# Kernel tuning notes

Hardware: AMD Instinct MI355X
Metric: run time of the kernel (lower is better)

Reference implementation:

```python
import jax, jax.numpy as jnp
import numpy as np
from jax import lax

C = 64          # grid_channels
RGB = 3         # rgb_channels
D = 128         # conditioning_dim
NUM_CLASSES = 1000
HIDDEN = 256    # hypernet hidden
NUM_STEPS = 32
TOT1 = C * C * 9


def setup_inputs() -> dict:
    key = jax.random.key(0)
    ks = jax.random.split(key, 20)
    s = 0.02
    B, H, W = 32, 64, 64
    return {
        "class_labels": jax.random.randint(ks[0], (B,), 0, NUM_CLASSES),
        "initial_grid": jax.random.normal(ks[1], (B, C, H, W), jnp.float32) * 0.1,
        "emb": jax.random.normal(ks[2], (NUM_CLASSES, D), jnp.float32) * s,
        "hw1": jax.random.normal(ks[3], (D, HIDDEN), jnp.float32) * s,
        "hb1": jnp.zeros((HIDDEN,), jnp.float32),
        "hw2": jax.random.normal(ks[4], (HIDDEN, HIDDEN), jnp.float32) * s,
        "hb2": jnp.zeros((HIDDEN,), jnp.float32),
        "hw3": jax.random.normal(ks[5], (HIDDEN, 2 * TOT1), jnp.float32) * s,
        "hb3": jnp.zeros((2 * TOT1,), jnp.float32),
        "f1w1": jax.random.normal(ks[6], (D, D), jnp.float32) * s,
        "f1b1": jnp.zeros((D,), jnp.float32),
        "f1w2": jax.random.normal(ks[7], (D, 2 * C), jnp.float32) * s,
        "f1b2": jnp.concatenate([jnp.ones((C,), jnp.float32), jnp.zeros((C,), jnp.float32)]),
        "f2w1": jax.random.normal(ks[8], (D, D), jnp.float32) * s,
        "f2b1": jnp.zeros((D,), jnp.float32),
        "f2w2": jax.random.normal(ks[9], (D, 2 * C), jnp.float32) * s,
        "f2b2": jnp.concatenate([jnp.ones((C,), jnp.float32), jnp.zeros((C,), jnp.float32)]),
        "blend": jnp.float32(0.5),
    }


def _conv_circ_one(x, w):
    # x: [C,H,W], w: [Cout,Cin,3,3]; circular pad then VALID conv == padding=1 circular
    xp = jnp.pad(x, ((0, 0), (1, 1), (1, 1)), mode='wrap')
    return lax.conv_general_dilated(xp[None], w, (1, 1), 'VALID')[0]

_bconv = jax.vmap(_conv_circ_one)  # per-sample dynamic weights over batch


def _film_params(cond, w1, b1, w2, b2):
    p = jax.nn.relu(cond @ w1 + b1) @ w2 + b2  # [B, 2C]
    return p[:, :C, None, None], p[:, C:, None, None]


def reference(class_labels, initial_grid, emb, hw1, hb1, hw2, hb2, hw3, hb3,
              f1w1, f1b1, f1w2, f1b2, f2w1, f2b1, f2w2, f2b2, blend):
    cond = emb[class_labels]                       # [B, D]
    h = jax.nn.relu(cond @ hw1 + hb1)
    h = jax.nn.relu(h @ hw2 + hb2)
    weights = h @ hw3 + hb3                        # [B, 2*C*C*9]
    B = cond.shape[0]
    w1 = weights[:, :TOT1].reshape(B, C, C, 3, 3)
    w2 = weights[:, TOT1:].reshape(B, C, C, 3, 3)
    g1, be1 = _film_params(cond, f1w1, f1b1, f1w2, f1b2)
    g2, be2 = _film_params(cond, f2w1, f2b1, f2w2, f2b2)
    blend_s = jax.nn.sigmoid(blend)

    def step(grid, _):
        u = jax.nn.relu(g1 * _bconv(grid, w1) + be1)
        u = jax.nn.relu(g2 * _bconv(u, w2) + be2)
        grid = (1 - blend_s) * grid + blend_s * u
        rgb = jax.nn.sigmoid(grid[:, :RGB])
        return grid, rgb

    _, traj = lax.scan(step, initial_grid, None, length=NUM_STEPS)  # [T,B,3,H,W]
    return traj[-1], traj
```

## Files before the change

kernel.cpp:

```cpp
#include <hip/hip_runtime.h>


typedef __attribute__((ext_vector_type(8))) short short8;
typedef __attribute__((ext_vector_type(4))) float f32x4;
typedef __attribute__((ext_vector_type(8))) unsigned short us8;

__device__ __forceinline__ unsigned short f2bf(float f) {
  unsigned int u = __builtin_bit_cast(unsigned int, f);
  u = (u + 0x7FFFu + ((u >> 16) & 1u)) >> 16;
  return (unsigned short)u;
}
__device__ __forceinline__ float bf2f(unsigned short h) {
  unsigned int u = ((unsigned int)h) << 16;
  return __builtin_bit_cast(float, u);
}

__device__ __forceinline__ void gl_lds16(const void* g, void* l) {
  __builtin_amdgcn_global_load_lds((const __attribute__((address_space(1))) void*)g,
                                   (__attribute__((address_space(3))) void*)l, 16, 0, 0);
}

__global__ void hyper_kernel(const int* __restrict__ labels, const float* __restrict__ emb,
                             const float* __restrict__ hw1, const float* __restrict__ hb1,
                             const float* __restrict__ hw2, const float* __restrict__ hb2,
                             float* __restrict__ h2T) {
  __shared__ float cond[128];
  __shared__ float h1[256];
  const int s = blockIdx.x, j = threadIdx.x;
  if (j < 128) cond[j] = emb[(size_t)labels[s] * 128 + j];
  __syncthreads();
  float a = hb1[j];
  for (int k = 0; k < 128; ++k) a += cond[k] * hw1[k * 256 + j];
  h1[j] = fmaxf(a, 0.f);
  __syncthreads();
  float a2 = hb2[j];
  for (int k = 0; k < 256; ++k) a2 += h1[k] * hw2[k * 256 + j];
  h2T[j * 32 + s] = fmaxf(a2, 0.f);
}

__global__ void film_kernel(const int* __restrict__ labels, const float* __restrict__ emb,
                            const float* __restrict__ f1w1, const float* __restrict__ f1b1,
                            const float* __restrict__ f1w2, const float* __restrict__ f1b2,
                            const float* __restrict__ f2w1, const float* __restrict__ f2b1,
                            const float* __restrict__ f2w2, const float* __restrict__ f2b2,
                            float* __restrict__ film) {
  __shared__ float cond[128];
  __shared__ float hid[128];
  const int s = blockIdx.x, which = blockIdx.y, j = threadIdx.x;
  const float* W1 = which ? f2w1 : f1w1;
  const float* B1 = which ? f2b1 : f1b1;
  const float* W2 = which ? f2w2 : f1w2;
  const float* B2 = which ? f2b2 : f1b2;
  cond[j] = emb[(size_t)labels[s] * 128 + j];
  __syncthreads();
  float a = B1[j];
  for (int k = 0; k < 128; ++k) a += cond[k] * W1[k * 128 + j];
  hid[j] = fmaxf(a, 0.f);
  __syncthreads();
  float p = B2[j];
  for (int k = 0; k < 128; ++k) p += hid[k] * W2[k * 128 + j];
  film[(size_t)((which * 2 + (j >> 6)) * 32 + s) * 64 + (j & 63)] = p;
}

__launch_bounds__(256)
__global__ void wgen_kernel(const float* __restrict__ h2T, const float* __restrict__ hw3,
                            const float* __restrict__ hb3, unsigned short* __restrict__ W) {
  __shared__ float h2l[8192];
  const int t = threadIdx.x;
  for (int i = t; i < 8192; i += 256) h2l[i] = h2T[i];
  __syncthreads();
  const int j  = blockIdx.x * 64 + (t & 63);
  const int sg = t >> 6;
  float acc[8];
  #pragma unroll
  for (int i = 0; i < 8; ++i) acc[i] = 0.f;
  const float* hp = &h2l[sg * 8];
  #pragma unroll 4
  for (int k = 0; k < 256; ++k) {
    const float w = hw3[(size_t)k * 73728 + j];
    const float4 hA = *(const float4*)(hp + k * 32);
    const float4 hB = *(const float4*)(hp + k * 32 + 4);
    acc[0] += hA.x * w; acc[1] += hA.y * w; acc[2] += hA.z * w; acc[3] += hA.w * w;
    acc[4] += hB.x * w; acc[5] += hB.y * w; acc[6] += hB.z * w; acc[7] += hB.w * w;
  }
  const float bias = hb3[j];
  const int cv = j / 36864;
  const int r  = j - cv * 36864;
  const int co = r / 576;
  const int r2 = r - co * 576;
  const int ci = r2 / 9;
  const int tap = r2 - ci * 9;
  const int sw = (co * 64 + ci) ^ ((co & 7) << 3);
  #pragma unroll
  for (int i = 0; i < 8; ++i) {
    const int s2 = sg * 8 + i;
    W[(size_t)((s2 * 2 + cv) * 9 + tap) * 4096 + sw] = f2bf(acc[i] + bias);
  }
}

__global__ void init_kernel(const float* __restrict__ gin, unsigned short* __restrict__ g0) {
  __shared__ float lds[64][65];
  const int b = blockIdx.x >> 6, y = blockIdx.x & 63;
  const int t = threadIdx.x;
  {
    const int ci = t >> 2, xq = t & 3;
    const float* base = gin + (size_t)((b * 64 + ci) * 64 + y) * 64;
    #pragma unroll
    for (int q = 0; q < 4; ++q) {
      const int x0 = (xq + q * 4) * 4;
      const float4 v = *(const float4*)(base + x0);
      lds[ci][x0+0] = v.x; lds[ci][x0+1] = v.y; lds[ci][x0+2] = v.z; lds[ci][x0+3] = v.w;
    }
  }
  __syncthreads();
  const int x = t >> 2, cq = t & 3, ci0 = cq * 16;
  us8 lo, hi;
  #pragma unroll
  for (int i = 0; i < 8; ++i) lo[i] = f2bf(lds[ci0 + i][x]);
  #pragma unroll
  for (int i = 0; i < 8; ++i) hi[i] = f2bf(lds[ci0 + 8 + i][x]);
  char* dbase = (char*)(g0 + (size_t)(b * 64 + y) * 4096);
  const int o = x * 128 + ci0 * 2, sw = (x & 7) << 4;
  *(us8*)(dbase + (o ^ sw)) = lo;
  *(us8*)(dbase + ((o + 16) ^ sw)) = hi;
}

template<int WHICH>
__launch_bounds__(512, 2)
__global__ void conv_kernel(const unsigned short* __restrict__ Wall,
                            const unsigned short* __restrict__ src,
                            unsigned short* __restrict__ dst,
                            const unsigned short* __restrict__ gold,
                            const float* __restrict__ film,
                            const float* __restrict__ blendp,
                            float* __restrict__ out, int t) {
  __shared__ unsigned short in_lds[10 * 4096];
  __shared__ unsigned short w_lds[9 * 4096];
  const int tid  = threadIdx.x;
  const int wid  = tid >> 6;
  const int lane = tid & 63;
  const int l15  = lane & 15;
  const int lhi  = lane >> 4;
  const int s    = blockIdx.x >> 3;
  const int y0   = (blockIdx.x & 7) * 8;

  const unsigned short* srcs = src + (size_t)s * 262144;
  const unsigned short* Wb   = Wall + (size_t)((s * 2 + WHICH) * 9) * 4096;

  #pragma unroll
  for (int q = 0; q < 10; ++q) {
    const int c   = q * 8 + wid;
    const int row = c >> 3, part = c & 7;
    const int gy  = (y0 + row + 63) & 63;
    gl_lds16(srcs + gy * 4096 + part * 512 + lane * 8, &in_lds[row * 4096 + part * 512]);
  }
  #pragma unroll
  for (int q = 0; q < 9; ++q) {
    const int c = q * 8 + wid;
    gl_lds16(Wb + c * 512 + lane * 8, &w_lds[c * 512]);
  }
  asm volatile("s_waitcnt vmcnt(0)" ::: "memory");
  __syncthreads();

  f32x4 acc[4][4];
  #pragma unroll
  for (int m = 0; m < 4; ++m)
    #pragma unroll
    for (int n = 0; n < 4; ++n)
      #pragma unroll
      for (int j = 0; j < 4; ++j) acc[m][n][j] = 0.f;

  #pragma unroll
  for (int tap = 0; tap < 9; ++tap) {
    const int ky = tap / 3, kx = tap % 3;
    short8 af[4][2], bfr[4][2];
    #pragma unroll
    for (int m = 0; m < 4; ++m) {
      const int co = m * 16 + l15;
      #pragma unroll
      for (int kk = 0; kk < 2; ++kk) {
        const int off = tap * 8192 + ((co * 128 + kk * 64 + lhi * 16) ^ ((co & 7) << 4));
        af[m][kk] = *(const short8*)((const char*)w_lds + off);
      }
    }
    const int r = wid + ky;
    #pragma unroll
    for (int n = 0; n < 4; ++n) {
      const int xs = (n * 16 + l15 + kx + 63) & 63;
      #pragma unroll
      for (int kk = 0; kk < 2; ++kk) {
        const int off = r * 8192 + ((xs * 128 + kk * 64 + lhi * 16) ^ ((xs & 7) << 4));
        bfr[n][kk] = *(const short8*)((const char*)in_lds + off);
      }
    }
    #pragma unroll
    for (int kk = 0; kk < 2; ++kk)
      #pragma unroll
      for (int m = 0; m < 4; ++m)
        #pragma unroll
        for (int n = 0; n < 4; ++n)
          acc[m][n] = __builtin_amdgcn_mfma_f32_16x16x32_bf16(af[m][kk], bfr[n][kk], acc[m][n], 0, 0, 0);
  }

  const int y = y0 + wid;
  const float* fg = film + WHICH * 2 * 2048;
  const float* fb = fg + 2048;
  float bs = 0.f, obs = 0.f;
  if (WHICH == 1) { bs = 1.f / (1.f + expf(-blendp[0])); obs = 1.f - bs; }
  unsigned short* drow = dst + (size_t)s * 262144 + y * 4096;
  const unsigned short* grow = (WHICH == 1) ? (gold + (size_t)s * 262144 + y * 4096) : (const unsigned short*)nullptr;

  #pragma unroll
  for (int m = 0; m < 4; ++m) {
    const int co0 = m * 16 + lhi * 4;
    const float4 g  = *(const float4*)&fg[s * 64 + co0];
    const float4 be = *(const float4*)&fb[s * 64 + co0];
    #pragma unroll
    for (int n = 0; n < 4; ++n) {
      const int x = n * 16 + l15;
      const int off = (x * 128 + co0 * 2) ^ ((x & 7) << 4);
      const f32x4 v = acc[m][n];
      const float u0 = fmaxf(g.x * v[0] + be.x, 0.f);
      const float u1 = fmaxf(g.y * v[1] + be.y, 0.f);
      const float u2 = fmaxf(g.z * v[2] + be.z, 0.f);
      const float u3 = fmaxf(g.w * v[3] + be.w, 0.f);
      if (WHICH == 0) {
        ushort4 pk; pk.x = f2bf(u0); pk.y = f2bf(u1); pk.z = f2bf(u2); pk.w = f2bf(u3);
        *(ushort4*)((char*)drow + off) = pk;
      } else {
        const ushort4 od = *(const ushort4*)((const char*)grow + off);
        const float g0 = obs * bf2f(od.x) + bs * u0;
        const float g1 = obs * bf2f(od.y) + bs * u1;
        const float g2 = obs * bf2f(od.z) + bs * u2;
        const float g3 = obs * bf2f(od.w) + bs * u3;
        ushort4 pk; pk.x = f2bf(g0); pk.y = f2bf(g1); pk.z = f2bf(g2); pk.w = f2bf(g3);
        *(ushort4*)((char*)drow + off) = pk;
        if (co0 == 0) {
          const float r0 = 1.f / (1.f + expf(-g0));
          const float r1 = 1.f / (1.f + expf(-g1));
          const float r2 = 1.f / (1.f + expf(-g2));
          float* ob = out + 393216 + (size_t)((t * 32 + s) * 3) * 4096 + y * 64 + x;
          ob[0] = r0; ob[4096] = r1; ob[8192] = r2;
          if (t == 31) {
            float* o2 = out + (size_t)(s * 3) * 4096 + y * 64 + x;
            o2[0] = r0; o2[4096] = r1; o2[8192] = r2;
          }
        }
      }
    }
  }
}

extern "C" void kernel_launch(void* const* d_in, const int* in_sizes, int n_in,
                              void* d_out, int out_size, void* d_ws, size_t ws_size,
                              hipStream_t stream) {
  (void)in_sizes; (void)n_in; (void)out_size; (void)ws_size;
  const int*   labels = (const int*)d_in[0];
  const float* gin    = (const float*)d_in[1];
  const float* emb    = (const float*)d_in[2];
  const float* hw1    = (const float*)d_in[3];
  const float* hb1    = (const float*)d_in[4];
  const float* hw2    = (const float*)d_in[5];
  const float* hb2    = (const float*)d_in[6];
  const float* hw3    = (const float*)d_in[7];
  const float* hb3    = (const float*)d_in[8];
  const float* f1w1   = (const float*)d_in[9];
  const float* f1b1   = (const float*)d_in[10];
  const float* f1w2   = (const float*)d_in[11];
  const float* f1b2   = (const float*)d_in[12];
  const float* f2w1   = (const float*)d_in[13];
  const float* f2b1   = (const float*)d_in[14];
  const float* f2w2   = (const float*)d_in[15];
  const float* f2b2   = (const float*)d_in[16];
  const float* blend  = (const float*)d_in[17];
  float* out = (float*)d_out;

  char* ws = (char*)d_ws;
  unsigned short* grid0 = (unsigned short*)(ws + (size_t)0);
  unsigned short* grid1 = (unsigned short*)(ws + (size_t)16777216);
  unsigned short* ubuf  = (unsigned short*)(ws + (size_t)33554432);
  unsigned short* Wbuf  = (unsigned short*)(ws + (size_t)50331648);
  float* h2T  = (float*)(ws + (size_t)55050240);
  float* film = (float*)(ws + (size_t)55083008);

  hyper_kernel<<<32, 256, 0, stream>>>(labels, emb, hw1, hb1, hw2, hb2, h2T);
  film_kernel<<<dim3(32, 2), 128, 0, stream>>>(labels, emb, f1w1, f1b1, f1w2, f1b2,
                                               f2w1, f2b1, f2w2, f2b2, film);
  wgen_kernel<<<1152, 256, 0, stream>>>(h2T, hw3, hb3, Wbuf);
  init_kernel<<<2048, 256, 0, stream>>>(gin, grid0);

  for (int t = 0; t < 32; ++t) {
    unsigned short* gi = (t & 1) ? grid1 : grid0;
    unsigned short* go = (t & 1) ? grid0 : grid1;
    conv_kernel<0><<<256, 512, 0, stream>>>(Wbuf, gi, ubuf, nullptr, film, nullptr, nullptr, t);
    conv_kernel<1><<<256, 512, 0, stream>>>(Wbuf, ubuf, go, gi, film, blend, out, t);
  }
}
```

Measured before the change: 1.430 ms.

## Double-buffer conv tap fragments, software-pipeline wgen loads, remap conv block order

The conv kernel now loads the LDS fragments for the next tap into a second register set while MFMAs run on the current tap, and raises wave priority around the MFMA block. The wgen kernel has each thread compute two output columns with float2 loads and a four-deep register prefetch of hw3 rows, which halves the grid size. Conv blocks are also remapped so that consecutive block IDs cover different samples instead of different row bands of one sample. The register pressure from the extra fragment buffers could reduce occupancy under the 512x2 launch bounds.

```diff
diff --git a/kernel.cpp b/kernel.cpp
--- a/kernel.cpp
+++ b/kernel.cpp
@@ -69,32 +69,78 @@
   const int t = threadIdx.x;
   for (int i = t; i < 8192; i += 256) h2l[i] = h2T[i];
   __syncthreads();
-  const int j  = blockIdx.x * 64 + (t & 63);
-  const int sg = t >> 6;
-  float acc[8];
-  #pragma unroll
-  for (int i = 0; i < 8; ++i) acc[i] = 0.f;
-  const float* hp = &h2l[sg * 8];
-  #pragma unroll 4
-  for (int k = 0; k < 256; ++k) {
-    const float w = hw3[(size_t)k * 73728 + j];
-    const float4 hA = *(const float4*)(hp + k * 32);
-    const float4 hB = *(const float4*)(hp + k * 32 + 4);
-    acc[0] += hA.x * w; acc[1] += hA.y * w; acc[2] += hA.z * w; acc[3] += hA.w * w;
-    acc[4] += hB.x * w; acc[5] += hB.y * w; acc[6] += hB.z * w; acc[7] += hB.w * w;
-  }
-  const float bias = hb3[j];
-  const int cv = j / 36864;
-  const int r  = j - cv * 36864;
-  const int co = r / 576;
-  const int r2 = r - co * 576;
-  const int ci = r2 / 9;
-  const int tap = r2 - ci * 9;
-  const int sw = (co * 64 + ci) ^ ((co & 7) << 3);
-  #pragma unroll
-  for (int i = 0; i < 8; ++i) {
-    const int s2 = sg * 8 + i;
-    W[(size_t)((s2 * 2 + cv) * 9 + tap) * 4096 + sw] = f2bf(acc[i] + bias);
+  const int lane = t & 63, sg = t >> 6;
+  const int j0 = blockIdx.x * 128 + lane * 2;
+  const float* __restrict__ gp = hw3 + j0;
+  const float* __restrict__ hp = h2l + sg * 8;
+
+  float acc[16];
+  #pragma unroll
+  for (int i = 0; i < 16; ++i) acc[i] = 0.f;
+
+  float2 bA[8], bB[8], bC[8], bD[8];
+  #pragma unroll
+  for (int u = 0; u < 8; ++u) bA[u] = *(const float2*)(gp + (size_t)(u) * 73728);
+  #pragma unroll
+  for (int u = 0; u < 8; ++u) bB[u] = *(const float2*)(gp + (size_t)(8 + u) * 73728);
+  #pragma unroll
+  for (int u = 0; u < 8; ++u) bC[u] = *(const float2*)(gp + (size_t)(16 + u) * 73728);
+
+#define WG_COMPUTE(BUF, KB)                                                    \
+  _Pragma("unroll")                                                            \
+  for (int u = 0; u < 8; ++u) {                                                \
+    const float4 hA = *(const float4*)(hp + ((KB) + u) * 32);                  \
+    const float4 hB = *(const float4*)(hp + ((KB) + u) * 32 + 4);              \
+    const float2 wv = BUF[u];                                                  \
+    acc[0]  += hA.x * wv.x; acc[1]  += hA.x * wv.y;                            \
+    acc[2]  += hA.y * wv.x; acc[3]  += hA.y * wv.y;                            \
+    acc[4]  += hA.z * wv.x; acc[5]  += hA.z * wv.y;                            \
+    acc[6]  += hA.w * wv.x; acc[7]  += hA.w * wv.y;                            \
+    acc[8]  += hB.x * wv.x; acc[9]  += hB.x * wv.y;                            \
+    acc[10] += hB.y * wv.x; acc[11] += hB.y * wv.y;                            \
+    acc[12] += hB.z * wv.x; acc[13] += hB.z * wv.y;                            \
+    acc[14] += hB.w * wv.x; acc[15] += hB.w * wv.y;                            \
+  }
+
+  #pragma unroll 1
+  for (int kc = 0; kc < 256; kc += 32) {
+    #pragma unroll
+    for (int u = 0; u < 8; ++u) bD[u] = *(const float2*)(gp + (size_t)(kc + 24 + u) * 73728);
+    WG_COMPUTE(bA, kc)
+    if (kc < 224) {
+      #pragma unroll
+      for (int u = 0; u < 8; ++u) bA[u] = *(const float2*)(gp + (size_t)(kc + 32 + u) * 73728);
+    }
+    WG_COMPUTE(bB, kc + 8)
+    if (kc < 224) {
+      #pragma unroll
+      for (int u = 0; u < 8; ++u) bB[u] = *(const float2*)(gp + (size_t)(kc + 40 + u) * 73728);
+    }
+    WG_COMPUTE(bC, kc + 16)
+    if (kc < 224) {
+      #pragma unroll
+      for (int u = 0; u < 8; ++u) bC[u] = *(const float2*)(gp + (size_t)(kc + 48 + u) * 73728);
+    }
+    WG_COMPUTE(bD, kc + 24)
+  }
+#undef WG_COMPUTE
+
+  #pragma unroll
+  for (int c = 0; c < 2; ++c) {
+    const int j  = j0 + c;
+    const float bias = hb3[j];
+    const int cv = j / 36864;
+    const int r  = j - cv * 36864;
+    const int co = r / 576;
+    const int r2 = r - co * 576;
+    const int ci = r2 / 9;
+    const int tap = r2 - ci * 9;
+    const int sw = (co * 64 + ci) ^ ((co & 7) << 3);
+    #pragma unroll
+    for (int i = 0; i < 8; ++i) {
+      const int s2 = sg * 8 + i;
+      W[(size_t)((s2 * 2 + cv) * 9 + tap) * 4096 + sw] = f2bf(acc[i * 2 + c] + bias);
+    }
   }
 }
 
@@ -141,8 +187,9 @@
   const int lane = tid & 63;
   const int l15  = lane & 15;
   const int lhi  = lane >> 4;
-  const int s    = blockIdx.x >> 3;
-  const int y0   = (blockIdx.x & 7) * 8;
+  const int b    = blockIdx.x;
+  const int s    = (b & 7) + 8 * ((b >> 3) & 3);
+  const int y0   = (b >> 5) * 8;
 
   const unsigned short* srcs = src + (size_t)s * 262144;
   const unsigned short* Wb   = Wall + (size_t)((s * 2 + WHICH) * 9) * 4096;
@@ -170,37 +217,58 @@
       #pragma unroll
       for (int j = 0; j < 4; ++j) acc[m][n][j] = 0.f;
 
-  #pragma unroll
-  for (int tap = 0; tap < 9; ++tap) {
-    const int ky = tap / 3, kx = tap % 3;
-    short8 af[4][2], bfr[4][2];
-    #pragma unroll
-    for (int m = 0; m < 4; ++m) {
-      const int co = m * 16 + l15;
-      #pragma unroll
-      for (int kk = 0; kk < 2; ++kk) {
-        const int off = tap * 8192 + ((co * 128 + kk * 64 + lhi * 16) ^ ((co & 7) << 4));
-        af[m][kk] = *(const short8*)((const char*)w_lds + off);
-      }
-    }
-    const int r = wid + ky;
-    #pragma unroll
-    for (int n = 0; n < 4; ++n) {
-      const int xs = (n * 16 + l15 + kx + 63) & 63;
-      #pragma unroll
-      for (int kk = 0; kk < 2; ++kk) {
-        const int off = r * 8192 + ((xs * 128 + kk * 64 + lhi * 16) ^ ((xs & 7) << 4));
-        bfr[n][kk] = *(const short8*)((const char*)in_lds + off);
-      }
-    }
-    #pragma unroll
-    for (int kk = 0; kk < 2; ++kk)
-      #pragma unroll
-      for (int m = 0; m < 4; ++m)
-        #pragma unroll
-        for (int n = 0; n < 4; ++n)
-          acc[m][n] = __builtin_amdgcn_mfma_f32_16x16x32_bf16(af[m][kk], bfr[n][kk], acc[m][n], 0, 0, 0);
-  }
+  short8 afA[4][2], bfA[4][2], afB[4][2], bfB[4][2];
+
+#define CONV_LOAD(AF, BF, TAP)                                                  \
+  {                                                                             \
+    const int ky = (TAP) / 3, kx = (TAP) % 3;                                   \
+    _Pragma("unroll")                                                           \
+    for (int m = 0; m < 4; ++m) {                                               \
+      const int co = m * 16 + l15;                                              \
+      _Pragma("unroll")                                                         \
+      for (int kk = 0; kk < 2; ++kk) {                                          \
+        const int off = (TAP) * 8192 +                                          \
+            ((co * 128 + kk * 64 + lhi * 16) ^ ((co & 7) << 4));                \
+        AF[m][kk] = *(const short8*)((const char*)w_lds + off);                 \
+      }                                                                         \
+    }                                                                           \
+    const int r = wid + ky;                                                     \
+    _Pragma("unroll")                                                           \
+    for (int n = 0; n < 4; ++n) {                                               \
+      const int xs = (n * 16 + l15 + kx + 63) & 63;                             \
+      _Pragma("unroll")                                                         \
+      for (int kk = 0; kk < 2; ++kk) {                                          \
+        const int off = r * 8192 +                                              \
+            ((xs * 128 + kk * 64 + lhi * 16) ^ ((xs & 7) << 4));                \
+        BF[n][kk] = *(const short8*)((const char*)in_lds + off);                \
+      }                                                                         \
+    }                                                                           \
+  }
+
+#define CONV_MMAC(AF, BF)                                                       \
+  __builtin_amdgcn_s_setprio(1);                                                \
+  _Pragma("unroll")                                                             \
+  for (int kk = 0; kk < 2; ++kk)                                                \
+    _Pragma("unroll")                                                           \
+    for (int m = 0; m < 4; ++m)                                                 \
+      _Pragma("unroll")                                                         \
+      for (int n = 0; n < 4; ++n)                                               \
+        acc[m][n] = __builtin_amdgcn_mfma_f32_16x16x32_bf16(                    \
+            AF[m][kk], BF[n][kk], acc[m][n], 0, 0, 0);                          \
+  __builtin_amdgcn_s_setprio(0);
+
+  CONV_LOAD(afA, bfA, 0)
+  CONV_LOAD(afB, bfB, 1)  CONV_MMAC(afA, bfA)
+  CONV_LOAD(afA, bfA, 2)  CONV_MMAC(afB, bfB)
+  CONV_LOAD(afB, bfB, 3)  CONV_MMAC(afA, bfA)
+  CONV_LOAD(afA, bfA, 4)  CONV_MMAC(afB, bfB)
+  CONV_LOAD(afB, bfB, 5)  CONV_MMAC(afA, bfA)
+  CONV_LOAD(afA, bfA, 6)  CONV_MMAC(afB, bfB)
+  CONV_LOAD(afB, bfB, 7)  CONV_MMAC(afA, bfA)
+  CONV_LOAD(afA, bfA, 8)  CONV_MMAC(afB, bfB)
+  CONV_MMAC(afA, bfA)
+#undef CONV_LOAD
+#undef CONV_MMAC
 
   const int y = y0 + wid;
   const float* fg = film + WHICH * 2 * 2048;
@@ -286,7 +354,7 @@
   hyper_kernel<<<32, 256, 0, stream>>>(labels, emb, hw1, hb1, hw2, hb2, h2T);
   film_kernel<<<dim3(32, 2), 128, 0, stream>>>(labels, emb, f1w1, f1b1, f1w2, f1b2,
                                                f2w1, f2b1, f2w2, f2b2, film);
-  wgen_kernel<<<1152, 256, 0, stream>>>(h2T, hw3, hb3, Wbuf);
+  wgen_kernel<<<576, 256, 0, stream>>>(h2T, hw3, hb3, Wbuf);
   init_kernel<<<2048, 256, 0, stream>>>(gin, grid0);
 
   for (int t = 0; t < 32; ++t) {
```

New measurement: 1.234 ms. -13.7%, faster.
